# Performance work log

Hardware: AMD Instinct MI355X
Metric: run time of the kernel (lower is better)

## Reference

```python
import jax, jax.numpy as jnp
import numpy as np

T, H, I, E, K = 1024, 1024, 512, 32, 4   # tokens, hidden, moe_inter, n_experts, top_k
G, TG, NS = 8, 4, 2                      # n_group, topk_group, n_shared_experts
C = 2 * T * K // E                       # expert capacity (no-drop headroom)
SCALE = 2.5                              # routed_scaling_factor


def setup_inputs() -> dict:
    key = jax.random.key(0)
    ks = jax.random.split(key, 7)
    s = 0.02
    return dict(
        hidden_states=jax.random.normal(ks[0], (T, H), jnp.float32),
        gate_w=jax.random.normal(ks[1], (E, H), jnp.float32) * s,
        e_bias=jax.random.normal(ks[2], (E,), jnp.float32) * 0.1,
        w_gate_up=jax.random.normal(ks[3], (E, 2 * I, H), jnp.float32) * s,
        w_down=jax.random.normal(ks[4], (E, H, I), jnp.float32) * s,
        w_gate_up_shared=jax.random.normal(ks[5], (2 * I * NS, H), jnp.float32) * s,
        w_down_shared=jax.random.normal(ks[6], (H, I * NS), jnp.float32) * s,
    )


def reference(hidden_states, gate_w, e_bias, w_gate_up, w_down, w_gate_up_shared, w_down_shared):
    x = hidden_states                                   # (T, H)
    # --- gate + sigmoid scoring (noaux_tc) ---
    logits = x @ gate_w.T                               # (T, E)
    scores = jax.nn.sigmoid(logits.astype(jnp.float32))
    sfc = scores + e_bias                               # scores_for_choice
    # --- group-limited top-k: top-2 sum per group, keep topk_group groups ---
    group_scores = jax.lax.top_k(sfc.reshape(T, G, E // G), 2)[0].sum(-1)  # (T, G)
    grp_idx = jax.lax.top_k(group_scores, TG)[1]        # (T, TG)
    gmask = jnp.zeros((T, G), jnp.float32).at[jnp.arange(T)[:, None], grp_idx].set(1.0)
    smask = jnp.repeat(gmask, E // G, axis=1)           # (T, E)
    sfc_m = jnp.where(smask > 0, sfc, 0.0)
    topk_idx = jax.lax.top_k(sfc_m, K)[1]               # (T, K)
    tw = jnp.take_along_axis(scores, topk_idx, axis=1)  # weights from raw scores
    tw = tw / (tw.sum(-1, keepdims=True) + 1e-20)       # norm_topk_prob
    tw = tw * SCALE
    # --- capacity-based dispatch (position within expert via cumsum of one-hot) ---
    e_flat = topk_idx.reshape(-1)                       # (T*K,)
    oh = jax.nn.one_hot(e_flat, E, dtype=jnp.float32)   # (T*K, E)
    pos = jnp.sum((jnp.cumsum(oh, axis=0) - 1.0) * oh, axis=-1).astype(jnp.int32)
    keep = (pos < C).astype(jnp.float32)                # capacity sized to never drop
    pos_c = jnp.clip(pos, 0, C - 1)
    t_flat = jnp.repeat(jnp.arange(T), K)
    combine = jnp.zeros((T, E, C), jnp.float32).at[t_flat, e_flat, pos_c].add(tw.reshape(-1) * keep)
    dispatch = jnp.zeros((T, E, C), jnp.float32).at[t_flat, e_flat, pos_c].add(keep)
    # --- grouped expert MLP (gate_up -> SiluAndMul -> down) ---
    xe = jnp.einsum('tec,th->ech', dispatch, x)         # (E, C, H)
    gu = jnp.einsum('ech,eoh->eco', xe, w_gate_up)      # (E, C, 2I)
    act = jax.nn.silu(gu[..., :I]) * gu[..., I:]
    ye = jnp.einsum('eci,ehi->ech', act, w_down)        # (E, C, H)
    routed = jnp.einsum('tec,ech->th', combine, ye)     # (T, H)
    # --- shared experts MLP on residual ---
    IS = I * NS
    gus = x @ w_gate_up_shared.T                        # (T, 2*IS)
    acts = jax.nn.silu(gus[:, :IS]) * gus[:, IS:]
    shared = acts @ w_down_shared.T                     # (T, H)
    return routed + shared
```

## Files before the change

### kernel.cpp

```cpp
#include <hip/hip_runtime.h>
#include <hip/hip_bf16.h>
#include <math.h>

#define T_TOK 1024
#define H_DIM 1024
#define I_DIM 512
#define E_NUM 32
#define K_TOP 4
#define G_NUM 8
#define TG_NUM 4
#define CAP 256
#define IS_DIM 1024
#define RSCALE 2.5f

#define MAXTILES 72

#define WS_CNT_OFF    0
#define WS_NT_OFF     128
#define WS_TILE_OFF   256
#define WS_EIDX_OFF   4096
#define WS_WN_OFF     20480
#define WS_STOK_OFF   36864
#define WS_SW_OFF     69632
#define WS_ACT_OFF    102400
#define WS_ACTS_OFF   (102400 + (size_t)E_NUM*CAP*I_DIM*2)
#define WS_XB_OFF     (WS_ACTS_OFF + (size_t)T_TOK*IS_DIM*2)
#define WS_T2S_OFF    (WS_XB_OFF + (size_t)T_TOK*H_DIM*2)
#define WS_YR_OFF     (WS_T2S_OFF + (size_t)T_TOK*K_TOP*4)

typedef __attribute__((ext_vector_type(8))) short short8v;
typedef __attribute__((ext_vector_type(4))) float f32x4;
typedef __attribute__((ext_vector_type(4))) unsigned uint4v;

__device__ __forceinline__ short f2bf(float f) {
    unsigned u = __float_as_uint(f);
    u += 0x7FFFu + ((u >> 16) & 1u);
    return (short)(u >> 16);
}
__device__ __forceinline__ unsigned pk2bf(float a, float b) {
    unsigned ua = __float_as_uint(a) + 0x8000u;
    unsigned ub = __float_as_uint(b) + 0x8000u;
    return __builtin_amdgcn_perm(ub, ua, 0x07060302);
}
__device__ __forceinline__ uint4v pk8bf(float4 lo, float4 hi) {
    uint4v r; r.x = pk2bf(lo.x, lo.y); r.y = pk2bf(lo.z, lo.w);
    r.z = pk2bf(hi.x, hi.y); r.w = pk2bf(hi.z, hi.w); return r;
}
__device__ __forceinline__ float silu_(float g) { return g / (1.f + expf(-g)); }

#define BAR_RELAXED() do { \
    asm volatile("s_waitcnt lgkmcnt(0)" ::: "memory"); \
    __builtin_amdgcn_s_barrier(); \
    asm volatile("" ::: "memory"); \
} while (0)

#define LDSTRIDE 72

__global__ __launch_bounds__(256) void gate_kernel(
    const float* __restrict__ x, const float* __restrict__ gate_w,
    const float* __restrict__ e_bias,
    int* __restrict__ eidx, float* __restrict__ wnorm, short* __restrict__ xb)
{
    __shared__ float xs[H_DIM];
    __shared__ float logits[E_NUM];
    const int t = blockIdx.x;
    const int tid = threadIdx.x;
    float4 v = ((const float4*)(x + (size_t)t * H_DIM))[tid];
    ((float4*)xs)[tid] = v;
    {
        unsigned* xd = (unsigned*)(xb + (size_t)t * H_DIM) + tid * 2;
        xd[0] = pk2bf(v.x, v.y); xd[1] = pk2bf(v.z, v.w);
    }
    __syncthreads();

    const int e = tid >> 3, sub = tid & 7;
    const float4* gw4 = (const float4*)(gate_w + (size_t)e * H_DIM + sub * 128);
    const float4* xr4 = (const float4*)(xs + sub * 128);
    float p = 0.f;
    #pragma unroll
    for (int h = 0; h < 32; ++h) {
        float4 a = xr4[h], b = gw4[h];
        p += a.x * b.x + a.y * b.y + a.z * b.z + a.w * b.w;
    }
    for (int off = 4; off; off >>= 1) p += __shfl_down(p, off, 8);
    if (sub == 0) logits[e] = p;
    __syncthreads();
    if (tid != 0) return;

    float sc[E_NUM], sfc[E_NUM];
    for (int i = 0; i < E_NUM; ++i) {
        sc[i] = 1.f / (1.f + expf(-logits[i]));
        sfc[i] = sc[i] + e_bias[i];
    }
    float gs[G_NUM];
    for (int g = 0; g < G_NUM; ++g) {
        float m1 = -1e30f, m2 = -1e30f;
        for (int j = 0; j < E_NUM / G_NUM; ++j) {
            float v2 = sfc[g * (E_NUM / G_NUM) + j];
            if (v2 > m1) { m2 = m1; m1 = v2; } else if (v2 > m2) m2 = v2;
        }
        gs[g] = m1 + m2;
    }
    bool gm[G_NUM];
    for (int g = 0; g < G_NUM; ++g) gm[g] = false;
    for (int it = 0; it < TG_NUM; ++it) {
        int best = -1; float bv = -1e30f;
        for (int g = 0; g < G_NUM; ++g) if (!gm[g] && gs[g] > bv) { bv = gs[g]; best = g; }
        gm[best] = true;
    }
    float sm[E_NUM];
    for (int i = 0; i < E_NUM; ++i) sm[i] = gm[i / (E_NUM / G_NUM)] ? sfc[i] : 0.0f;
    int idx[K_TOP]; float w[K_TOP]; float tsum = 0.f;
    for (int it = 0; it < K_TOP; ++it) {
        int best = 0; float bv = -1e30f;
        for (int i = 0; i < E_NUM; ++i) if (sm[i] > bv) { bv = sm[i]; best = i; }
        sm[best] = -1e30f;
        idx[it] = best; w[it] = sc[best]; tsum += w[it];
    }
    float inv = RSCALE / (tsum + 1e-20f);
    const int base = t * K_TOP;
    for (int it = 0; it < K_TOP; ++it) {
        eidx[base + it] = idx[it];
        wnorm[base + it] = w[it] * inv;
    }
}

__global__ __launch_bounds__(1024) void assign_kernel(
    const int* __restrict__ eidx, const float* __restrict__ wnorm,
    int* __restrict__ cnt, int* __restrict__ slot_token, float* __restrict__ slot_w,
    int* __restrict__ ntiles, int* __restrict__ tiles, int* __restrict__ tok2slot)
{
    __shared__ int   se[T_TOK * K_TOP];
    __shared__ float swt[T_TOK * K_TOP];
    __shared__ int   scnt[E_NUM];
    const int tid = threadIdx.x;
    for (int i = tid; i < T_TOK * K_TOP; i += 1024) { se[i] = eidx[i]; swt[i] = wnorm[i]; }
    __syncthreads();

    const int e = tid >> 5;
    const int seg = tid & 31;
    const int base = seg * 128;
    int c = 0;
    for (int i = 0; i < 128; ++i) c += (se[base + i] == e);
    int excl = 0, total = 0;
    for (int s = 0; s < 32; ++s) {
        int cs = __shfl(c, s, 32);
        total += cs;
        if (s < seg) excl += cs;
    }
    if (seg == 0) { cnt[e] = total; scnt[e] = total; }
    __syncthreads();
    int boff = 0;
    for (int ee = 0; ee < e; ++ee) boff += min(scnt[ee], CAP);

    int pos = excl;
    for (int i = 0; i < 128; ++i) {
        if (se[base + i] == e) {
            const int g = base + i;
            if (pos < CAP) {
                slot_token[e * CAP + pos] = g >> 2;
                slot_w[e * CAP + pos] = swt[g];
                tok2slot[g] = boff + pos;
            } else {
                tok2slot[g] = -1;
            }
            ++pos;
        }
    }
    __syncthreads();
    if (tid == 0) {
        int nt = 0;
        for (int t0 = 0; t0 < T_TOK; t0 += 128) {
            tiles[nt * 4] = -1; tiles[nt * 4 + 1] = t0; tiles[nt * 4 + 2] = 128;
            tiles[nt * 4 + 3] = 0; ++nt;
        }
        int off = 0;
        for (int ee = 0; ee < E_NUM; ++ee) {
            int n = min(scnt[ee], CAP);
            for (int r = 0; r < n; r += 128) {
                tiles[nt * 4] = ee; tiles[nt * 4 + 1] = r;
                tiles[nt * 4 + 2] = min(128, n - r);
                tiles[nt * 4 + 3] = off + r; ++nt;
            }
            off += n;
        }
        *ntiles = nt;
    }
}


#define GEMM_SETUP() \
    const int tid = threadIdx.x; \
    const int lane = tid & 63, wid = tid >> 6; \
    const int wm = wid & 1, wn = wid >> 1; \
    const int lr16 = lane & 15, kc = lane >> 4; \
    const int sc_ = tid & 7, srow = tid >> 3; \
    const int aoff0 = srow * LDSTRIDE + sc_ * 8; \
    const int aoff1 = (srow + 64) * LDSTRIDE + sc_ * 8;

#define DECL_ACC42() f32x4 acc[4][2]; \
    _Pragma("unroll") for (int i_ = 0; i_ < 4; ++i_) \
    _Pragma("unroll") for (int j_ = 0; j_ < 2; ++j_) acc[i_][j_] = 0.f;

#define COMPUTE_BK64(Asb, Bsb) do { \
    _Pragma("unroll") for (int ks = 0; ks < 2; ++ks) { \
        short8v a_[4], b_[2]; \
        _Pragma("unroll") for (int mt = 0; mt < 4; ++mt) \
            a_[mt] = *(const short8v*)&(Asb)[(wm*64 + mt*16 + lr16)*LDSTRIDE + ks*32 + kc*8]; \
        _Pragma("unroll") for (int nt = 0; nt < 2; ++nt) \
            b_[nt] = *(const short8v*)&(Bsb)[(wn*32 + nt*16 + lr16)*LDSTRIDE + ks*32 + kc*8]; \
        _Pragma("unroll") for (int mt = 0; mt < 4; ++mt) \
        _Pragma("unroll") for (int nt = 0; nt < 2; ++nt) \
            acc[mt][nt] = __builtin_amdgcn_mfma_f32_16x16x32_bf16(a_[mt], b_[nt], acc[mt][nt], 0, 0, 0); \
    } \
} while (0)

#define LOAD_SET(A0, A1, B0a, B0b, B1a, B1b, KOFF) do { \
    A0 = *(const short8v*)(aptr0 + (KOFF)); \
    A1 = *(const short8v*)(aptr1 + (KOFF)); \
    B0a = *(const float4*)(bptr0 + (KOFF)); B0b = *(const float4*)(bptr0 + (KOFF) + 4); \
    B1a = *(const float4*)(bptr1 + (KOFF)); B1b = *(const float4*)(bptr1 + (KOFF) + 4); \
} while (0)

#define STAGE_SET(A0, A1, B0a, B0b, B1a, B1b, BUF) do { \
    *(short8v*)&As[BUF][aoff0] = A0; \
    *(short8v*)&As[BUF][aoff1] = A1; \
    *(uint4v*)&Bs[BUF][aoff0]  = pk8bf(B0a, B0b); \
    *(uint4v*)&Bs[BUF][aoff1]  = pk8bf(B1a, B1b); \
} while (0)

#define PIPE_BODY(KDIM) \
    short8v pA0, pA1, qA0, qA1; \
    float4 pB0a, pB0b, pB1a, pB1b, qB0a, qB0b, qB1a, qB1b; \
    LOAD_SET(pA0, pA1, pB0a, pB0b, pB1a, pB1b, 0); \
    LOAD_SET(qA0, qA1, qB0a, qB0b, qB1a, qB1b, 64); \
    int buf = 0; \
    for (int k0 = 0; k0 < (KDIM); k0 += 128) { \
        STAGE_SET(pA0, pA1, pB0a, pB0b, pB1a, pB1b, buf); \
        if (k0 + 128 < (KDIM)) LOAD_SET(pA0, pA1, pB0a, pB0b, pB1a, pB1b, k0 + 128); \
        BAR_RELAXED(); \
        COMPUTE_BK64(As[buf], Bs[buf]); \
        buf ^= 1; \
        STAGE_SET(qA0, qA1, qB0a, qB0b, qB1a, qB1b, buf); \
        if (k0 + 192 < (KDIM)) LOAD_SET(qA0, qA1, qB0a, qB0b, qB1a, qB1b, k0 + 192); \
        BAR_RELAXED(); \
        COMPUTE_BK64(As[buf], Bs[buf]); \
        buf ^= 1; \
    }

__global__ __launch_bounds__(512, 2) void gu_all_kernel(
    const short* __restrict__ xb, const float* __restrict__ w_gate_up,
    const float* __restrict__ w_gus,
    const int* __restrict__ ntiles, const int* __restrict__ tiles,
    const int* __restrict__ slot_token, const float* __restrict__ slot_w,
    short* __restrict__ act, short* __restrict__ acts)
{
    if ((int)blockIdx.y >= *ntiles) return;
    const int e  = tiles[blockIdx.y * 4];
    const int r0 = tiles[blockIdx.y * 4 + 1];
    const int ne = tiles[blockIdx.y * 4 + 2];
    const bool sh = (e < 0);
    if (!sh && blockIdx.x >= I_DIM / 64) return;
    const int col0 = blockIdx.x * 64;

    __shared__ __align__(16) short As[2][128 * LDSTRIDE];
    __shared__ __align__(16) short Bs[2][128 * LDSTRIDE];
    __shared__ int   toks[128];
    __shared__ float sws[128];

    GEMM_SETUP();
    if (tid < 128) {
        if (sh) { toks[tid] = r0 + tid; sws[tid] = 1.f; }
        else {
            bool v = tid < ne;
            toks[tid] = v ? slot_token[e * CAP + r0 + tid] : 0;
            sws[tid]  = v ? slot_w[e * CAP + r0 + tid] : 0.f;
        }
    }
    __syncthreads();

    const int IDim = sh ? IS_DIM : I_DIM;
    const float* wbase = sh ? w_gus : (w_gate_up + (size_t)e * (2 * I_DIM) * H_DIM);
    const int r_0 = srow, r_1 = srow + 64;
    const int wr0 = ((r_0 >> 4) & 1) * IDim + col0 + ((r_0 >> 5) << 4) + (r_0 & 15);
    const int wr1 = ((r_1 >> 4) & 1) * IDim + col0 + ((r_1 >> 5) << 4) + (r_1 & 15);
    const float* bptr0 = wbase + (size_t)wr0 * H_DIM + sc_ * 8;
    const float* bptr1 = wbase + (size_t)wr1 * H_DIM + sc_ * 8;
    const short* aptr0 = xb + (size_t)toks[r_0] * H_DIM + sc_ * 8;
    const short* aptr1 = xb + (size_t)toks[r_1] * H_DIM + sc_ * 8;

    DECL_ACC42();
    PIPE_BODY(H_DIM);

    #pragma unroll
    for (int mt = 0; mt < 4; ++mt) {
        f32x4 g = acc[mt][0], u = acc[mt][1];
        const int colI = col0 + wn * 16 + lr16;
        #pragma unroll
        for (int i = 0; i < 4; ++i) {
            int r = wm * 64 + mt * 16 + kc * 4 + i;
            if (r < ne) {
                float s = sws[r];
                short* dst = sh ? (acts + (size_t)(r0 + r) * IS_DIM + colI)
                                : (act + ((size_t)e * CAP + r0 + r) * I_DIM + colI);
                *dst = f2bf(s * silu_(g[i]) * u[i]);
            }
        }
    }
}

__global__ __launch_bounds__(512, 2) void down_all_kernel(
    const short* __restrict__ act, const short* __restrict__ acts,
    const float* __restrict__ w_down, const float* __restrict__ w_ds,
    const int* __restrict__ ntiles, const int* __restrict__ tiles,
    float* __restrict__ yr, float* __restrict__ out)
{
    if ((int)blockIdx.y >= *ntiles) return;
    const int e  = tiles[blockIdx.y * 4];
    const int r0 = tiles[blockIdx.y * 4 + 1];
    const int ne = tiles[blockIdx.y * 4 + 2];
    const int bo = tiles[blockIdx.y * 4 + 3];
    const bool sh = (e < 0);
    const int h0 = blockIdx.x * 128;

    __shared__ __align__(16) short As[2][128 * LDSTRIDE];
    __shared__ __align__(16) short Bs[2][128 * LDSTRIDE];

    GEMM_SETUP();

    const int Kdim = sh ? IS_DIM : I_DIM;
    const short* abase = sh ? (acts + (size_t)r0 * IS_DIM)
                            : (act + ((size_t)e * CAP + r0) * I_DIM);
    const float* wbase = sh ? w_ds : (w_down + (size_t)e * H_DIM * I_DIM);
    const float* bptr0 = wbase + (size_t)(h0 + srow) * Kdim + sc_ * 8;
    const float* bptr1 = wbase + (size_t)(h0 + srow + 64) * Kdim + sc_ * 8;
    const short* aptr0 = abase + (size_t)srow * Kdim + sc_ * 8;
    const short* aptr1 = abase + (size_t)(srow + 64) * Kdim + sc_ * 8;

    DECL_ACC42();
    PIPE_BODY(Kdim);

    #pragma unroll
    for (int mt = 0; mt < 4; ++mt) {
        #pragma unroll
        for (int i = 0; i < 4; ++i) {
            int r = wm * 64 + mt * 16 + kc * 4 + i;
            if (r < ne) {
                float* orow = sh ? (out + (size_t)(r0 + r) * H_DIM + h0 + wn * 32)
                                 : (yr + (size_t)(bo + r) * H_DIM + h0 + wn * 32);
                #pragma unroll
                for (int nt = 0; nt < 2; ++nt)
                    orow[nt * 16 + lr16] = acc[mt][nt][i];
            }
        }
    }
}

__global__ __launch_bounds__(256) void combine_kernel(
    const float* __restrict__ yr, const int* __restrict__ tok2slot,
    float* __restrict__ out)
{
    const int t = blockIdx.x, tid = threadIdx.x;
    float4 a = ((const float4*)(out + (size_t)t * H_DIM))[tid];
    #pragma unroll
    for (int k = 0; k < K_TOP; ++k) {
        int s = tok2slot[t * K_TOP + k];
        if (s >= 0) {
            float4 b = ((const float4*)(yr + (size_t)s * H_DIM))[tid];
            a.x += b.x; a.y += b.y; a.z += b.z; a.w += b.w;
        }
    }
    ((float4*)(out + (size_t)t * H_DIM))[tid] = a;
}

extern "C" void kernel_launch(void* const* d_in, const int* in_sizes, int n_in,
                              void* d_out, int out_size, void* d_ws, size_t ws_size,
                              hipStream_t stream) {
    const float* x   = (const float*)d_in[0];
    const float* gw  = (const float*)d_in[1];
    const float* eb  = (const float*)d_in[2];
    const float* wgu = (const float*)d_in[3];
    const float* wd  = (const float*)d_in[4];
    const float* wgs = (const float*)d_in[5];
    const float* wds = (const float*)d_in[6];
    float* out = (float*)d_out;
    char* ws = (char*)d_ws;

    int*   cnt    = (int*)(ws + WS_CNT_OFF);
    int*   ntiles = (int*)(ws + WS_NT_OFF);
    int*   tiles  = (int*)(ws + WS_TILE_OFF);
    int*   eidx   = (int*)(ws + WS_EIDX_OFF);
    float* wnorm  = (float*)(ws + WS_WN_OFF);
    int*   stok   = (int*)(ws + WS_STOK_OFF);
    float* sw     = (float*)(ws + WS_SW_OFF);
    short* act    = (short*)(ws + WS_ACT_OFF);
    short* acts   = (short*)(ws + WS_ACTS_OFF);
    short* xb     = (short*)(ws + WS_XB_OFF);
    int*   t2s    = (int*)(ws + WS_T2S_OFF);
    float* yr     = (float*)(ws + WS_YR_OFF);

    gate_kernel<<<T_TOK, 256, 0, stream>>>(x, gw, eb, eidx, wnorm, xb);
    assign_kernel<<<1, 1024, 0, stream>>>(eidx, wnorm, cnt, stok, sw, ntiles, tiles, t2s);
    gu_all_kernel<<<dim3(IS_DIM / 64, MAXTILES), 512, 0, stream>>>(
        xb, wgu, wgs, ntiles, tiles, stok, sw, act, acts);
    down_all_kernel<<<dim3(H_DIM / 128, MAXTILES), 512, 0, stream>>>(
        act, acts, wd, wds, ntiles, tiles, yr, out);
    combine_kernel<<<T_TOK, 256, 0, stream>>>(yr, t2s, out);
}
```

Baseline: 416.3 us.

## Shrink GEMM M-tile to 64 rows and simplify pipeline for higher occupancy

Halves the row tile of the gate-up and down GEMMs from 128 to 64 tokens, doubling the tile count and cutting accumulators per wave to 2x2. The pipeline drops the two-set prefetch unroll for a single-stage register prefetch over 64-wide K, and launch bounds now ask for 6 blocks per SM. The LDS stride changes from 72 to 68. The aim is to cut padding waste on partly filled expert tiles and raise occupancy and parallelism. The cost is that each weight tile is now loaded and converted to bf16 by twice as many blocks. Stride 68 may also cause LDS bank conflicts or break 16-byte alignment of the vector LDS accesses, and down_all_kernel gains an unused toks array plus an extra barrier.

```diff
diff --git a/kernel.cpp b/kernel.cpp
--- a/kernel.cpp
+++ b/kernel.cpp
@@ -13,7 +13,7 @@
 #define IS_DIM 1024
 #define RSCALE 2.5f
 
-#define MAXTILES 72
+#define MAXTILES 160
 
 #define WS_CNT_OFF    0
 #define WS_NT_OFF     128
@@ -54,7 +54,7 @@
     asm volatile("" ::: "memory"); \
 } while (0)
 
-#define LDSTRIDE 72
+#define LDSTRIDE 68
 
 __global__ __launch_bounds__(256) void gate_kernel(
     const float* __restrict__ x, const float* __restrict__ gate_w,
@@ -170,16 +170,16 @@
     __syncthreads();
     if (tid == 0) {
         int nt = 0;
-        for (int t0 = 0; t0 < T_TOK; t0 += 128) {
-            tiles[nt * 4] = -1; tiles[nt * 4 + 1] = t0; tiles[nt * 4 + 2] = 128;
+        for (int t0 = 0; t0 < T_TOK; t0 += 64) {
+            tiles[nt * 4] = -1; tiles[nt * 4 + 1] = t0; tiles[nt * 4 + 2] = 64;
             tiles[nt * 4 + 3] = 0; ++nt;
         }
         int off = 0;
         for (int ee = 0; ee < E_NUM; ++ee) {
             int n = min(scnt[ee], CAP);
-            for (int r = 0; r < n; r += 128) {
+            for (int r = 0; r < n; r += 64) {
                 tiles[nt * 4] = ee; tiles[nt * 4 + 1] = r;
-                tiles[nt * 4 + 2] = min(128, n - r);
+                tiles[nt * 4 + 2] = min(64, n - r);
                 tiles[nt * 4 + 3] = off + r; ++nt;
             }
             off += n;
@@ -195,60 +195,50 @@
     const int wm = wid & 1, wn = wid >> 1; \
     const int lr16 = lane & 15, kc = lane >> 4; \
     const int sc_ = tid & 7, srow = tid >> 3; \
-    const int aoff0 = srow * LDSTRIDE + sc_ * 8; \
-    const int aoff1 = (srow + 64) * LDSTRIDE + sc_ * 8;
-
-#define DECL_ACC42() f32x4 acc[4][2]; \
-    _Pragma("unroll") for (int i_ = 0; i_ < 4; ++i_) \
+    const int aoff  = srow * LDSTRIDE + sc_ * 8; \
+    const int boff1 = (srow + 64) * LDSTRIDE + sc_ * 8;
+
+#define DECL_ACC22() f32x4 acc[2][2]; \
+    _Pragma("unroll") for (int i_ = 0; i_ < 2; ++i_) \
     _Pragma("unroll") for (int j_ = 0; j_ < 2; ++j_) acc[i_][j_] = 0.f;
 
 #define COMPUTE_BK64(Asb, Bsb) do { \
     _Pragma("unroll") for (int ks = 0; ks < 2; ++ks) { \
-        short8v a_[4], b_[2]; \
-        _Pragma("unroll") for (int mt = 0; mt < 4; ++mt) \
-            a_[mt] = *(const short8v*)&(Asb)[(wm*64 + mt*16 + lr16)*LDSTRIDE + ks*32 + kc*8]; \
+        short8v a_[2], b_[2]; \
+        _Pragma("unroll") for (int mt = 0; mt < 2; ++mt) \
+            a_[mt] = *(const short8v*)&(Asb)[(wm*32 + mt*16 + lr16)*LDSTRIDE + ks*32 + kc*8]; \
         _Pragma("unroll") for (int nt = 0; nt < 2; ++nt) \
             b_[nt] = *(const short8v*)&(Bsb)[(wn*32 + nt*16 + lr16)*LDSTRIDE + ks*32 + kc*8]; \
-        _Pragma("unroll") for (int mt = 0; mt < 4; ++mt) \
+        _Pragma("unroll") for (int mt = 0; mt < 2; ++mt) \
         _Pragma("unroll") for (int nt = 0; nt < 2; ++nt) \
             acc[mt][nt] = __builtin_amdgcn_mfma_f32_16x16x32_bf16(a_[mt], b_[nt], acc[mt][nt], 0, 0, 0); \
     } \
 } while (0)
 
-#define LOAD_SET(A0, A1, B0a, B0b, B1a, B1b, KOFF) do { \
-    A0 = *(const short8v*)(aptr0 + (KOFF)); \
-    A1 = *(const short8v*)(aptr1 + (KOFF)); \
-    B0a = *(const float4*)(bptr0 + (KOFF)); B0b = *(const float4*)(bptr0 + (KOFF) + 4); \
-    B1a = *(const float4*)(bptr1 + (KOFF)); B1b = *(const float4*)(bptr1 + (KOFF) + 4); \
-} while (0)
-
-#define STAGE_SET(A0, A1, B0a, B0b, B1a, B1b, BUF) do { \
-    *(short8v*)&As[BUF][aoff0] = A0; \
-    *(short8v*)&As[BUF][aoff1] = A1; \
-    *(uint4v*)&Bs[BUF][aoff0]  = pk8bf(B0a, B0b); \
-    *(uint4v*)&Bs[BUF][aoff1]  = pk8bf(B1a, B1b); \
-} while (0)
-
 #define PIPE_BODY(KDIM) \
-    short8v pA0, pA1, qA0, qA1; \
-    float4 pB0a, pB0b, pB1a, pB1b, qB0a, qB0b, qB1a, qB1b; \
-    LOAD_SET(pA0, pA1, pB0a, pB0b, pB1a, pB1b, 0); \
-    LOAD_SET(qA0, qA1, qB0a, qB0b, qB1a, qB1b, 64); \
+    short8v cA = *(const short8v*)(aptr0); \
+    float4 cB0a = *(const float4*)(bptr0), cB0b = *(const float4*)(bptr0 + 4); \
+    float4 cB1a = *(const float4*)(bptr1), cB1b = *(const float4*)(bptr1 + 4); \
     int buf = 0; \
-    for (int k0 = 0; k0 < (KDIM); k0 += 128) { \
-        STAGE_SET(pA0, pA1, pB0a, pB0b, pB1a, pB1b, buf); \
-        if (k0 + 128 < (KDIM)) LOAD_SET(pA0, pA1, pB0a, pB0b, pB1a, pB1b, k0 + 128); \
+    for (int k0 = 0; k0 < (KDIM); k0 += 64) { \
+        short8v nA{}; \
+        float4 nB0a{}, nB0b{}, nB1a{}, nB1b{}; \
+        const int k1 = k0 + 64; \
+        if (k1 < (KDIM)) { \
+            nA = *(const short8v*)(aptr0 + k1); \
+            nB0a = *(const float4*)(bptr0 + k1); nB0b = *(const float4*)(bptr0 + k1 + 4); \
+            nB1a = *(const float4*)(bptr1 + k1); nB1b = *(const float4*)(bptr1 + k1 + 4); \
+        } \
+        *(short8v*)&As[buf][aoff] = cA; \
+        *(uint4v*)&Bs[buf][aoff]  = pk8bf(cB0a, cB0b); \
+        *(uint4v*)&Bs[buf][boff1] = pk8bf(cB1a, cB1b); \
         BAR_RELAXED(); \
         COMPUTE_BK64(As[buf], Bs[buf]); \
         buf ^= 1; \
-        STAGE_SET(qA0, qA1, qB0a, qB0b, qB1a, qB1b, buf); \
-        if (k0 + 192 < (KDIM)) LOAD_SET(qA0, qA1, qB0a, qB0b, qB1a, qB1b, k0 + 192); \
-        BAR_RELAXED(); \
-        COMPUTE_BK64(As[buf], Bs[buf]); \
-        buf ^= 1; \
-    }
-
-__global__ __launch_bounds__(512, 2) void gu_all_kernel(
+        cA = nA; cB0a = nB0a; cB0b = nB0b; cB1a = nB1a; cB1b = nB1b; \
+    }
+
+__global__ __launch_bounds__(512, 6) void gu_all_kernel(
     const short* __restrict__ xb, const float* __restrict__ w_gate_up,
     const float* __restrict__ w_gus,
     const int* __restrict__ ntiles, const int* __restrict__ tiles,
@@ -263,13 +253,13 @@
     if (!sh && blockIdx.x >= I_DIM / 64) return;
     const int col0 = blockIdx.x * 64;
 
-    __shared__ __align__(16) short As[2][128 * LDSTRIDE];
+    __shared__ __align__(16) short As[2][64 * LDSTRIDE];
     __shared__ __align__(16) short Bs[2][128 * LDSTRIDE];
-    __shared__ int   toks[128];
-    __shared__ float sws[128];
+    __shared__ int   toks[64];
+    __shared__ float sws[64];
 
     GEMM_SETUP();
-    if (tid < 128) {
+    if (tid < 64) {
         if (sh) { toks[tid] = r0 + tid; sws[tid] = 1.f; }
         else {
             bool v = tid < ne;
@@ -286,19 +276,18 @@
     const int wr1 = ((r_1 >> 4) & 1) * IDim + col0 + ((r_1 >> 5) << 4) + (r_1 & 15);
     const float* bptr0 = wbase + (size_t)wr0 * H_DIM + sc_ * 8;
     const float* bptr1 = wbase + (size_t)wr1 * H_DIM + sc_ * 8;
-    const short* aptr0 = xb + (size_t)toks[r_0] * H_DIM + sc_ * 8;
-    const short* aptr1 = xb + (size_t)toks[r_1] * H_DIM + sc_ * 8;
-
-    DECL_ACC42();
+    const short* aptr0 = xb + (size_t)toks[srow] * H_DIM + sc_ * 8;
+
+    DECL_ACC22();
     PIPE_BODY(H_DIM);
 
     #pragma unroll
-    for (int mt = 0; mt < 4; ++mt) {
+    for (int mt = 0; mt < 2; ++mt) {
         f32x4 g = acc[mt][0], u = acc[mt][1];
         const int colI = col0 + wn * 16 + lr16;
         #pragma unroll
         for (int i = 0; i < 4; ++i) {
-            int r = wm * 64 + mt * 16 + kc * 4 + i;
+            int r = wm * 32 + mt * 16 + kc * 4 + i;
             if (r < ne) {
                 float s = sws[r];
                 short* dst = sh ? (acts + (size_t)(r0 + r) * IS_DIM + colI)
@@ -309,7 +298,7 @@
     }
 }
 
-__global__ __launch_bounds__(512, 2) void down_all_kernel(
+__global__ __launch_bounds__(512, 6) void down_all_kernel(
     const short* __restrict__ act, const short* __restrict__ acts,
     const float* __restrict__ w_down, const float* __restrict__ w_ds,
     const int* __restrict__ ntiles, const int* __restrict__ tiles,
@@ -323,10 +312,16 @@
     const bool sh = (e < 0);
     const int h0 = blockIdx.x * 128;
 
-    __shared__ __align__(16) short As[2][128 * LDSTRIDE];
+    __shared__ __align__(16) short As[2][64 * LDSTRIDE];
     __shared__ __align__(16) short Bs[2][128 * LDSTRIDE];
+    __shared__ int toks[64];
 
     GEMM_SETUP();
+    if (tid < 64) {
+        if (sh) toks[tid] = r0 + tid;
+        else    toks[tid] = 0;
+    }
+    __syncthreads();
 
     const int Kdim = sh ? IS_DIM : I_DIM;
     const short* abase = sh ? (acts + (size_t)r0 * IS_DIM)
@@ -335,16 +330,15 @@
     const float* bptr0 = wbase + (size_t)(h0 + srow) * Kdim + sc_ * 8;
     const float* bptr1 = wbase + (size_t)(h0 + srow + 64) * Kdim + sc_ * 8;
     const short* aptr0 = abase + (size_t)srow * Kdim + sc_ * 8;
-    const short* aptr1 = abase + (size_t)(srow + 64) * Kdim + sc_ * 8;
-
-    DECL_ACC42();
+
+    DECL_ACC22();
     PIPE_BODY(Kdim);
 
     #pragma unroll
-    for (int mt = 0; mt < 4; ++mt) {
+    for (int mt = 0; mt < 2; ++mt) {
         #pragma unroll
         for (int i = 0; i < 4; ++i) {
-            int r = wm * 64 + mt * 16 + kc * 4 + i;
+            int r = wm * 32 + mt * 16 + kc * 4 + i;
             if (r < ne) {
                 float* orow = sh ? (out + (size_t)(r0 + r) * H_DIM + h0 + wn * 32)
                                  : (yr + (size_t)(bo + r) * H_DIM + h0 + wn * 32);
```

Measured after the change: 425.3 us. +2.2%, slower.
